# Performance work log

Measured on AMD Instinct MI355X. Metric: run time of the kernel, lower is better.

Reference implementation:

```python
import jax, jax.numpy as jnp
import numpy as np

B_SZ = 1
SEQ = 4096
IN_DIM = 1024
D_MODEL = 512
D_INNER = 1024   # expand(2) * d_model
D_STATE = 16
D_CONV = 4
DT_RANK = 32     # ceil(d_model / 16)
N_LAYERS = 2
N_CLASSES = 2


def setup_inputs() -> dict:
    key = jax.random.key(0)
    ks = jax.random.split(key, 12)
    s = 0.02
    x = jax.random.normal(ks[0], (B_SZ, SEQ, IN_DIM), jnp.float32)
    fc1_w = jax.random.normal(ks[1], (D_MODEL, IN_DIM), jnp.float32) * s
    fc1_b = jnp.zeros((D_MODEL,), jnp.float32)
    ln_w = jnp.ones((N_LAYERS, D_MODEL), jnp.float32)
    ln_b = jnp.zeros((N_LAYERS, D_MODEL), jnp.float32)
    in_proj_w = jax.random.normal(ks[2], (N_LAYERS, 2 * D_INNER, D_MODEL), jnp.float32) * s
    conv_w = jax.random.normal(ks[3], (N_LAYERS, D_INNER, D_CONV), jnp.float32) * 0.1
    conv_b = jnp.zeros((N_LAYERS, D_INNER), jnp.float32)
    x_proj_w = jax.random.normal(ks[4], (N_LAYERS, DT_RANK + 2 * D_STATE, D_INNER), jnp.float32) * s
    dt_proj_w = jax.random.normal(ks[5], (N_LAYERS, D_INNER, DT_RANK), jnp.float32) * s
    # bias so softplus(bias) ~ 0.01 (typical dt init)
    dt_proj_b = jnp.full((N_LAYERS, D_INNER), float(np.log(np.expm1(0.01))), jnp.float32)
    A_log = jnp.broadcast_to(jnp.log(jnp.arange(1, D_STATE + 1, dtype=jnp.float32)),
                             (N_LAYERS, D_INNER, D_STATE)).copy()
    D_skip = jnp.ones((N_LAYERS, D_INNER), jnp.float32)
    norm_w = jnp.ones((D_MODEL,), jnp.float32)
    norm_b = jnp.zeros((D_MODEL,), jnp.float32)
    cls_w = jax.random.normal(ks[6], (N_CLASSES, D_MODEL), jnp.float32) * s
    cls_b = jnp.zeros((N_CLASSES,), jnp.float32)
    return {"x": x, "fc1_w": fc1_w, "fc1_b": fc1_b, "ln_w": ln_w, "ln_b": ln_b,
            "in_proj_w": in_proj_w, "conv_w": conv_w, "conv_b": conv_b,
            "x_proj_w": x_proj_w, "dt_proj_w": dt_proj_w, "dt_proj_b": dt_proj_b,
            "A_log": A_log, "D_skip": D_skip, "norm_w": norm_w, "norm_b": norm_b,
            "cls_w": cls_w, "cls_b": cls_b}


def layernorm(h, w, b, eps=1e-5):
    mu = h.mean(-1, keepdims=True)
    var = ((h - mu) ** 2).mean(-1, keepdims=True)
    return (h - mu) * jax.lax.rsqrt(var + eps) * w + b


def mamba_block(h, in_proj_w, conv_w, conv_b, x_proj_w, dt_proj_w, dt_proj_b, A_log, D_skip):
    # h: [B, L, d_model]
    xz = jnp.einsum('bld,ed->ble', h, in_proj_w)          # [B, L, 2*D_INNER]
    xc, z = jnp.split(xz, 2, axis=-1)                     # each [B, L, D_INNER]
    # causal depthwise conv along L (kernel D_CONV)
    xp = jnp.pad(xc, ((0, 0), (D_CONV - 1, 0), (0, 0)))
    conv = sum(xp[:, k:k + xc.shape[1], :] * conv_w[:, k] for k in range(D_CONV))
    xc = jax.nn.silu(conv + conv_b)
    dbc = jnp.einsum('bld,ed->ble', xc, x_proj_w)         # [B, L, DT_RANK + 2*N]
    dt = jax.nn.softplus(jnp.einsum('blr,dr->bld', dbc[..., :DT_RANK], dt_proj_w) + dt_proj_b)
    Bm = dbc[..., DT_RANK:DT_RANK + D_STATE]              # [B, L, N]
    Cm = dbc[..., DT_RANK + D_STATE:]                     # [B, L, N]
    A = -jnp.exp(A_log)                                   # [D_INNER, N]
    dA = jnp.exp(dt[..., None] * A)                       # [B, L, D_INNER, N]
    dBx = dt[..., None] * Bm[:, :, None, :] * xc[..., None]

    def step(s, ins):
        dA_t, dBx_t, C_t = ins
        s = dA_t * s + dBx_t                              # [B, D_INNER, N]
        y = jnp.einsum('bdn,bn->bd', s, C_t)
        return s, y

    s0 = jnp.zeros((h.shape[0], D_INNER, D_STATE), h.dtype)
    _, ys = jax.lax.scan(step, s0, (dA.transpose(1, 0, 2, 3),
                                    dBx.transpose(1, 0, 2, 3),
                                    Cm.transpose(1, 0, 2)))
    y = ys.transpose(1, 0, 2) + xc * D_skip               # [B, L, D_INNER]
    y = y * jax.nn.silu(z)
    return y


def reference(x, fc1_w, fc1_b, ln_w, ln_b, in_proj_w, conv_w, conv_b,
              x_proj_w, dt_proj_w, dt_proj_b, A_log, D_skip,
              norm_w, norm_b, cls_w, cls_b):
    # out_proj of each Mamba layer folded: out_proj_w stored in in_proj? No -> build here.
    # We use the last N_LAYERS rows trick not needed: out projection is d_inner->d_model,
    # reuse in_proj_w transposed halves would be unfaithful, so derive deterministic weights.
    out_proj_w = jnp.stack([
        jax.random.normal(jax.random.fold_in(jax.random.key(7), i),
                          (D_MODEL, D_INNER), jnp.float32) * 0.02
        for i in range(N_LAYERS)])
    h = jax.nn.gelu(jnp.einsum('bli,di->bld', x, fc1_w) + fc1_b)
    for i in range(N_LAYERS):
        res = h
        hn = layernorm(h, ln_w[i], ln_b[i])
        y = mamba_block(hn, in_proj_w[i], conv_w[i], conv_b[i], x_proj_w[i],
                        dt_proj_w[i], dt_proj_b[i], A_log[i], D_skip[i])
        h = jnp.einsum('ble,de->bld', y, out_proj_w[i]) + res
    h = layernorm(h, norm_w, norm_b)
    hidden = h.mean(axis=1)                               # avg aggregation
    pred = hidden @ cls_w.T + cls_b
    return hidden, pred, h
```

## Files before the change

kernel.cpp:

```cpp
#include <hip/hip_runtime.h>
#include <cstdint>
#include <cstddef>

#define SEQ     4096
#define IN_DIM  1024
#define D_MODEL 512
#define D_INNER 1024
#define D_STATE 16
#define DT_RANK 32

#define CHUNK   32
#define NCHUNK  128
#define NREC    16384

#define LOG2E 1.44269504088896f

static const size_t OFF_H     = 0;
static const size_t OFF_PS    = 2097152;
static const size_t OFF_Z     = 6291456;
static const size_t OFF_XC    = 10485760;
static const size_t OFF_DT    = 14680064;
static const size_t OFF_CARRY = 18874368;
static const size_t OFF_HNB   = 20971520;
static const size_t OFF_FC1WB = 22020096;
static const size_t OFF_WIB   = 22282240;
static const size_t OFF_XPWB  = 23330816;
static const size_t OFF_DPWB  = 23396352;
static const size_t OFF_DBCF  = 23429120;
static const size_t OFF_DBCB  = 23691264;
static const size_t OFF_WOUTB = 23822336;
static const size_t OFF_PART  = 24346624;

typedef __attribute__((ext_vector_type(8))) short bf16x8;
typedef __attribute__((ext_vector_type(4))) float f32x4;

__device__ __forceinline__ uint32_t rotl32(uint32_t v, int r) { return (v << r) | (v >> (32 - r)); }

__device__ __forceinline__ void threefry2x32(uint32_t k0, uint32_t k1, uint32_t x0, uint32_t x1,
                                             uint32_t& o0, uint32_t& o1) {
  uint32_t ks0 = k0, ks1 = k1, ks2 = k0 ^ k1 ^ 0x1BD11BDAu;
  x0 += ks0; x1 += ks1;
  const int rotA[4] = {13, 15, 26, 6};
  const int rotB[4] = {17, 29, 16, 24};
  uint32_t ks[3] = {ks0, ks1, ks2};
#pragma unroll
  for (int r = 0; r < 5; ++r) {
    const int* rr = (r & 1) ? rotB : rotA;
#pragma unroll
    for (int j = 0; j < 4; ++j) { x0 += x1; x1 = rotl32(x1, rr[j]); x1 ^= x0; }
    x0 += ks[(r + 1) % 3];
    x1 += ks[(r + 2) % 3] + (uint32_t)(r + 1);
  }
  o0 = x0; o1 = x1;
}

__device__ __forceinline__ float erfinv32(float x) {
  float w = -log1pf(-x * x);
  float p;
  if (w < 5.0f) {
    w -= 2.5f;
    p = 2.81022636e-08f;
    p = fmaf(p, w, 3.43273939e-07f);
    p = fmaf(p, w, -3.5233877e-06f);
    p = fmaf(p, w, -4.39150654e-06f);
    p = fmaf(p, w, 0.00021858087f);
    p = fmaf(p, w, -0.00125372503f);
    p = fmaf(p, w, -0.00417768164f);
    p = fmaf(p, w, 0.246640727f);
    p = fmaf(p, w, 1.50140941f);
  } else {
    w = sqrtf(w) - 3.0f;
    p = -0.000200214257f;
    p = fmaf(p, w, 0.000100950558f);
    p = fmaf(p, w, 0.00134934322f);
    p = fmaf(p, w, -0.00367342844f);
    p = fmaf(p, w, 0.00573950773f);
    p = fmaf(p, w, -0.0076224613f);
    p = fmaf(p, w, 0.00943887047f);
    p = fmaf(p, w, 1.00167406f);
    p = fmaf(p, w, 2.83297682f);
  }
  return p * x;
}

__device__ __forceinline__ float bits_to_normal(uint32_t b) {
  float f = __uint_as_float((b >> 9) | 0x3f800000u) - 1.0f;
  const float lo = -0.99999994f;
  float u = f * (1.0f - lo) + lo;
  u = fmaxf(lo, u);
  return 1.41421356f * erfinv32(u);
}

__device__ __forceinline__ ushort f2bf(float x) {
  uint32_t u = __float_as_uint(x);
  u = (u + 0x7FFFu + ((u >> 16) & 1u)) >> 16;
  return (ushort)u;
}
__device__ __forceinline__ bf16x8 pack8(float4 a, float4 b) {
  bf16x8 v;
  v[0] = f2bf(a.x); v[1] = f2bf(a.y); v[2] = f2bf(a.z); v[3] = f2bf(a.w);
  v[4] = f2bf(b.x); v[5] = f2bf(b.y); v[6] = f2bf(b.z); v[7] = f2bf(b.w);
  return v;
}

__global__ __launch_bounds__(256) void gen_wout(ushort* __restrict__ w) {
  int gid = blockIdx.x * 256 + threadIdx.x;
  int layer = gid >> 19;
  int j = gid & 0x7FFFF;
  uint32_t k0, k1;
  threefry2x32(0u, 7u, 0u, (uint32_t)layer, k0, k1);
  uint32_t o0, o1;
  threefry2x32(k0, k1, 0u, (uint32_t)j, o0, o1);
  w[(size_t)layer * 524288 + j] = f2bf(bits_to_normal(o0 ^ o1) * 0.02f);
}

__global__ __launch_bounds__(256) void convert_all(
    const float* __restrict__ x,   const float* __restrict__ fc1w,
    const float* __restrict__ ipw, const float* __restrict__ xpw,
    const float* __restrict__ dpw,
    ushort* __restrict__ xb, ushort* __restrict__ fc1wb, ushort* __restrict__ ipwb,
    ushort* __restrict__ xpwb, ushort* __restrict__ dpwb) {
  int gid = blockIdx.x * 256 + threadIdx.x;
  const float* src; ushort* dst; size_t off;
  if (gid < 524288)      { src = x;    dst = xb;    off = gid; }
  else if (gid < 589824) { src = fc1w; dst = fc1wb; off = gid - 524288; }
  else if (gid < 851968) { src = ipw;  dst = ipwb;  off = gid - 589824; }
  else if (gid < 868352) { src = xpw;  dst = xpwb;  off = gid - 851968; }
  else if (gid < 876544) { src = dpw;  dst = dpwb;  off = gid - 868352; }
  else return;
  const float4* p = (const float4*)(src + off * 8);
  *(bf16x8*)(dst + off * 8) = pack8(p[0], p[1]);
}

__device__ __forceinline__ float silu_f(float v) { return v / (1.0f + exp2f(-LOG2E * v)); }
__device__ __forceinline__ float gelu_f(float v) {
  float v3 = v * v * v;
  return 0.5f * v * (1.0f + tanhf(0.7978845608028654f * (v + 0.044715f * v3)));
}
__device__ __forceinline__ float softplus_f(float v) {
  return fmaxf(v, 0.0f) + log1pf(exp2f(-LOG2E * fabsf(v)));
}

enum { EPI_NONE = 0, EPI_BIAS_GELU = 1, EPI_INPROJ = 2, EPI_SOFTPLUS = 3, EPI_RESID = 4, EPI_DBC = 5 };

template <int EPI, int NT>
__global__ __launch_bounds__(256) void gemm_bf(
    const ushort* __restrict__ A, int lda,
    const ushort* __restrict__ B, int ldb,
    float* __restrict__ C, int ldc, int K,
    const float* __restrict__ bias, float* __restrict__ out2,
    ushort* __restrict__ outb) {
  constexpr int NB = NT / 64;
  __shared__ ushort As[2][64][40];
  __shared__ ushort Bs[2][NT][40];
  const int m0 = blockIdx.y * 64, n0 = blockIdx.x * NT;
  const int tid = threadIdx.x;
  const int arow = tid >> 2, ach = (tid & 3) * 8;
  const int lane = tid & 63, wid = tid >> 6;
  const int lr = lane & 15, lhi = lane >> 4;
  const ushort* Ap  = A + (size_t)(m0 + arow) * lda + ach;
  const ushort* Bp0 = B + (size_t)(n0 + arow) * ldb + ach;
  const ushort* Bp1 = (NB > 1) ? (B + (size_t)(n0 + 64 + arow) * ldb + ach) : Bp0;

  f32x4 acc[NT / 16] = {};
  uint4 ra, rb0, rb1;

  ra  = *(const uint4*)Ap;
  rb0 = *(const uint4*)Bp0;
  if (NB > 1) rb1 = *(const uint4*)Bp1;
  *(uint4*)&As[0][arow][ach] = ra;
  *(uint4*)&Bs[0][arow][ach] = rb0;
  if (NB > 1) *(uint4*)&Bs[0][64 + arow][ach] = rb1;
  __syncthreads();

  const int nk = K >> 5;
  int cur = 0;
  for (int ki = 0; ki < nk; ++ki) {
    const bool more = (ki + 1 < nk);
    if (more) {
      const int k = (ki + 1) << 5;
      ra  = *(const uint4*)(Ap + k);
      rb0 = *(const uint4*)(Bp0 + k);
      if (NB > 1) rb1 = *(const uint4*)(Bp1 + k);
    }
    bf16x8 af = *(const bf16x8*)&As[cur][wid * 16 + lr][lhi * 8];
#pragma unroll
    for (int t = 0; t < NT / 16; ++t) {
      bf16x8 bv = *(const bf16x8*)&Bs[cur][t * 16 + lr][lhi * 8];
      acc[t] = __builtin_amdgcn_mfma_f32_16x16x32_bf16(af, bv, acc[t], 0, 0, 0);
    }
    if (more) {
      *(uint4*)&As[cur ^ 1][arow][ach] = ra;
      *(uint4*)&Bs[cur ^ 1][arow][ach] = rb0;
      if (NB > 1) *(uint4*)&Bs[cur ^ 1][64 + arow][ach] = rb1;
    }
    __syncthreads();
    cur ^= 1;
  }

#pragma unroll
  for (int t = 0; t < NT / 16; ++t) {
    const int n = n0 + t * 16 + lr;
#pragma unroll
    for (int r = 0; r < 4; ++r) {
      const int m = m0 + wid * 16 + lhi * 4 + r;
      float v = acc[t][r];
      if (EPI == EPI_NONE) {
        C[(size_t)m * ldc + n] = v;
      } else if (EPI == EPI_BIAS_GELU) {
        v += bias[n];
        C[(size_t)m * ldc + n] = gelu_f(v);
      } else if (EPI == EPI_SOFTPLUS) {
        v += bias[n];
        C[(size_t)m * ldc + n] = softplus_f(v);
      } else if (EPI == EPI_RESID) {
        C[(size_t)m * ldc + n] += v;
      } else if (EPI == EPI_INPROJ) {
        if (n < D_INNER) C[(size_t)m * D_INNER + n] = v;
        else             out2[(size_t)m * D_INNER + (n - D_INNER)] = silu_f(v);
      } else if (EPI == EPI_DBC) {
        C[(size_t)m * 64 + n] = v;
        outb[(size_t)m * 64 + n] = f2bf(v);
      }
    }
  }
}

template <int EPI>
__global__ __launch_bounds__(256) void gemm_bf128(
    const ushort* __restrict__ A, int lda,
    const ushort* __restrict__ B, int ldb,
    float* __restrict__ C, int ldc, int K,
    const float* __restrict__ bias, float* __restrict__ out2) {
  __shared__ ushort As[2][128][40];
  __shared__ ushort Bs[2][128][40];
  const int m0 = blockIdx.y * 128, n0 = blockIdx.x * 128;
  const int tid = threadIdx.x;
  const int lane = tid & 63, wid = tid >> 6;
  const int lr = lane & 15, lhi = lane >> 4;
  const int r0_ = tid >> 2, ach = (tid & 3) * 8;
  const ushort* Ap0 = A + (size_t)(m0 + r0_) * lda + ach;
  const ushort* Ap1 = A + (size_t)(m0 + r0_ + 64) * lda + ach;
  const ushort* Bp0 = B + (size_t)(n0 + r0_) * ldb + ach;
  const ushort* Bp1 = B + (size_t)(n0 + r0_ + 64) * ldb + ach;

  f32x4 acc[16] = {};
  uint4 ra0, ra1, rb0, rb1;

  ra0 = *(const uint4*)Ap0; ra1 = *(const uint4*)Ap1;
  rb0 = *(const uint4*)Bp0; rb1 = *(const uint4*)Bp1;
  *(uint4*)&As[0][r0_][ach] = ra0; *(uint4*)&As[0][r0_ + 64][ach] = ra1;
  *(uint4*)&Bs[0][r0_][ach] = rb0; *(uint4*)&Bs[0][r0_ + 64][ach] = rb1;
  __syncthreads();

  const int nk = K >> 5;
  int cur = 0;
  for (int ki = 0; ki < nk; ++ki) {
    const bool more = (ki + 1 < nk);
    if (more) {
      const int k = (ki + 1) << 5;
      ra0 = *(const uint4*)(Ap0 + k); ra1 = *(const uint4*)(Ap1 + k);
      rb0 = *(const uint4*)(Bp0 + k); rb1 = *(const uint4*)(Bp1 + k);
    }
    bf16x8 af0 = *(const bf16x8*)&As[cur][wid * 32 + lr][lhi * 8];
    bf16x8 af1 = *(const bf16x8*)&As[cur][wid * 32 + 16 + lr][lhi * 8];
#pragma unroll
    for (int t = 0; t < 8; ++t) {
      bf16x8 bv = *(const bf16x8*)&Bs[cur][t * 16 + lr][lhi * 8];
      acc[t]     = __builtin_amdgcn_mfma_f32_16x16x32_bf16(af0, bv, acc[t], 0, 0, 0);
      acc[8 + t] = __builtin_amdgcn_mfma_f32_16x16x32_bf16(af1, bv, acc[8 + t], 0, 0, 0);
    }
    if (more) {
      *(uint4*)&As[cur ^ 1][r0_][ach] = ra0; *(uint4*)&As[cur ^ 1][r0_ + 64][ach] = ra1;
      *(uint4*)&Bs[cur ^ 1][r0_][ach] = rb0; *(uint4*)&Bs[cur ^ 1][r0_ + 64][ach] = rb1;
    }
    __syncthreads();
    cur ^= 1;
  }

#pragma unroll
  for (int fr = 0; fr < 2; ++fr) {
#pragma unroll
    for (int t = 0; t < 8; ++t) {
      const int n = n0 + t * 16 + lr;
#pragma unroll
      for (int r = 0; r < 4; ++r) {
        const int m = m0 + wid * 32 + fr * 16 + lhi * 4 + r;
        float v = acc[fr * 8 + t][r];
        if (EPI == EPI_INPROJ) {
          if (n < D_INNER) C[(size_t)m * D_INNER + n] = v;
          else             out2[(size_t)m * D_INNER + (n - D_INNER)] = silu_f(v);
        } else {
          C[(size_t)m * ldc + n] = v;
        }
      }
    }
  }
}

template <int BF>
__global__ __launch_bounds__(256) void ln_rows(const float* __restrict__ in,
                                               const float* __restrict__ w,
                                               const float* __restrict__ b,
                                               float* __restrict__ outf,
                                               ushort* __restrict__ outb) {
  __shared__ double red[4];
  const int row = blockIdx.x, t = threadIdx.x;
  const float* r = in + (size_t)row * D_MODEL;
  double x0 = (double)r[t], x1 = (double)r[t + 256];
  double s = x0 + x1;
#pragma unroll
  for (int o = 32; o >= 1; o >>= 1) s += __shfl_down(s, o);
  int wid = t >> 6, lane = t & 63;
  if (lane == 0) red[wid] = s;
  __syncthreads();
  double mu = (red[0] + red[1] + red[2] + red[3]) * (1.0 / 512.0);
  __syncthreads();
  double d0 = x0 - mu, d1 = x1 - mu;
  double v = d0 * d0 + d1 * d1;
#pragma unroll
  for (int o = 32; o >= 1; o >>= 1) v += __shfl_down(v, o);
  if (lane == 0) red[wid] = v;
  __syncthreads();
  double var = (red[0] + red[1] + red[2] + red[3]) * (1.0 / 512.0);
  double rs = rsqrt(var + 1e-5);
  float o0 = (float)(d0 * rs * (double)w[t] + (double)b[t]);
  float o1 = (float)(d1 * rs * (double)w[t + 256] + (double)b[t + 256]);
  if (BF) {
    outb[(size_t)row * D_MODEL + t]       = f2bf(o0);
    outb[(size_t)row * D_MODEL + t + 256] = f2bf(o1);
  } else {
    outf[(size_t)row * D_MODEL + t]       = o0;
    outf[(size_t)row * D_MODEL + t + 256] = o1;
  }
}

__global__ __launch_bounds__(256) void conv_silu2(const float* __restrict__ xcr,
                                                  const float* __restrict__ cw,
                                                  const float* __restrict__ cb,
                                                  float* __restrict__ outf,
                                                  ushort* __restrict__ outb) {
  const int l = blockIdx.x;
  for (int q = 0; q < 4; ++q) {
    const int d = threadIdx.x + q * 256;
    float acc = cb[d];
#pragma unroll
    for (int k = 0; k < 4; ++k) {
      const int ll = l + k - 3;
      const float xv = (ll >= 0) ? xcr[(size_t)ll * D_INNER + d] : 0.0f;
      acc = fmaf(xv, cw[d * 4 + k], acc);
    }
    float o = silu_f(acc);
    outf[(size_t)l * D_INNER + d] = o;
    outb[(size_t)l * D_INNER + d] = f2bf(o);
  }
}

__global__ __launch_bounds__(256) void scanA(const float* __restrict__ dt,
                                             const float* __restrict__ dbc,
                                             const float* __restrict__ xc,
                                             const float* __restrict__ Alog,
                                             float* __restrict__ P, float* __restrict__ S) {
  const int c = blockIdx.y;
  const int d = blockIdx.x * 256 + threadIdx.x;
  float a2[16], s[16];
#pragma unroll
  for (int q = 0; q < 4; ++q) {
    float4 al = *(const float4*)(Alog + (size_t)d * 16 + q * 4);
    a2[4*q+0] = -expf(al.x) * LOG2E; a2[4*q+1] = -expf(al.y) * LOG2E;
    a2[4*q+2] = -expf(al.z) * LOG2E; a2[4*q+3] = -expf(al.w) * LOG2E;
  }
#pragma unroll
  for (int n = 0; n < 16; ++n) s[n] = 0.0f;
  float sdt = 0.0f;
  const int l0 = c * CHUNK;
#pragma unroll 2
  for (int t = 0; t < CHUNK; ++t) {
    const int l = l0 + t;
    const float dtv = dt[(size_t)l * D_INNER + d];
    const float xv  = xc[(size_t)l * D_INNER + d];
    const float dx = dtv * xv;
    sdt += dtv;
    float bv[16];
    const float4* B4 = (const float4*)(dbc + (size_t)l * 64 + DT_RANK);
    *(float4*)&bv[0]  = B4[0]; *(float4*)&bv[4]  = B4[1];
    *(float4*)&bv[8]  = B4[2]; *(float4*)&bv[12] = B4[3];
#pragma unroll
    for (int n = 0; n < 16; ++n)
      s[n] = fmaf(exp2f(dtv * a2[n]), s[n], bv[n] * dx);
  }
  float4* Sp = (float4*)(S + (size_t)c * NREC + (size_t)d * 16);
  float4* Pp = (float4*)(P + (size_t)c * NREC + (size_t)d * 16);
#pragma unroll
  for (int q = 0; q < 4; ++q) {
    Sp[q] = make_float4(s[4*q], s[4*q+1], s[4*q+2], s[4*q+3]);
    Pp[q] = make_float4(exp2f(a2[4*q]*sdt), exp2f(a2[4*q+1]*sdt),
                        exp2f(a2[4*q+2]*sdt), exp2f(a2[4*q+3]*sdt));
  }
}

__global__ __launch_bounds__(256) void scanB(const float* __restrict__ P,
                                             const float* __restrict__ S,
                                             float* __restrict__ carry) {
  int idx = blockIdx.x * 256 + threadIdx.x;
  float cr = 0.0f;
  for (int c = 0; c < NCHUNK; ++c) {
    size_t k = (size_t)c * NREC + idx;
    carry[k] = cr;
    cr = fmaf(P[k], cr, S[k]);
  }
}

__global__ __launch_bounds__(256) void scanC(const float* __restrict__ dt,
                                             const float* __restrict__ dbc,
                                             const float* __restrict__ xc,
                                             const float* __restrict__ Alog,
                                             const float* __restrict__ carry,
                                             const float* __restrict__ Dskip,
                                             const float* __restrict__ zs,
                                             ushort* __restrict__ yb) {
  const int c = blockIdx.y;
  const int d = blockIdx.x * 256 + threadIdx.x;
  float a2[16], s[16];
#pragma unroll
  for (int q = 0; q < 4; ++q) {
    float4 al = *(const float4*)(Alog + (size_t)d * 16 + q * 4);
    a2[4*q+0] = -expf(al.x) * LOG2E; a2[4*q+1] = -expf(al.y) * LOG2E;
    a2[4*q+2] = -expf(al.z) * LOG2E; a2[4*q+3] = -expf(al.w) * LOG2E;
    float4 cr = *(const float4*)(carry + (size_t)c * NREC + (size_t)d * 16 + q * 4);
    s[4*q+0] = cr.x; s[4*q+1] = cr.y; s[4*q+2] = cr.z; s[4*q+3] = cr.w;
  }
  const float dsk = Dskip[d];
  const int l0 = c * CHUNK;
#pragma unroll 2
  for (int t = 0; t < CHUNK; ++t) {
    const int l = l0 + t;
    const float dtv = dt[(size_t)l * D_INNER + d];
    const float xv  = xc[(size_t)l * D_INNER + d];
    const float dx = dtv * xv;
    float bv[16], cv[16];
    const float4* B4 = (const float4*)(dbc + (size_t)l * 64 + DT_RANK);
    *(float4*)&bv[0]  = B4[0]; *(float4*)&bv[4]  = B4[1];
    *(float4*)&bv[8]  = B4[2]; *(float4*)&bv[12] = B4[3];
    *(float4*)&cv[0]  = B4[4]; *(float4*)&cv[4]  = B4[5];
    *(float4*)&cv[8]  = B4[6]; *(float4*)&cv[12] = B4[7];
    float acc = 0.0f;
#pragma unroll
    for (int n = 0; n < 16; ++n) {
      s[n] = fmaf(exp2f(dtv * a2[n]), s[n], bv[n] * dx);
      acc = fmaf(s[n], cv[n], acc);
    }
    float yv = fmaf(xv, dsk, acc);
    yb[(size_t)l * D_INNER + d] = f2bf(yv * zs[(size_t)l * D_INNER + d]);
  }
}

__global__ __launch_bounds__(512) void colsum(const float* __restrict__ h, double* __restrict__ part) {
  int d = threadIdx.x;
  int r0 = blockIdx.x * 128;
  double s = 0.0;
  for (int r = 0; r < 128; ++r) s += (double)h[(size_t)(r0 + r) * D_MODEL + d];
  part[blockIdx.x * D_MODEL + d] = s;
}

__global__ __launch_bounds__(512) void head_k(const double* __restrict__ part,
                                              const float* __restrict__ cls_w,
                                              const float* __restrict__ cls_b,
                                              float* __restrict__ out) {
  __shared__ double l0[512], l1[512];
  int d = threadIdx.x;
  double s = 0.0;
  for (int b = 0; b < 32; ++b) s += part[b * D_MODEL + d];
  double hv = s * (1.0 / 4096.0);
  out[d] = (float)hv;
  l0[d] = hv * (double)cls_w[d];
  l1[d] = hv * (double)cls_w[D_MODEL + d];
  __syncthreads();
  for (int o = 256; o > 0; o >>= 1) {
    if (d < o) { l0[d] += l0[d + o]; l1[d] += l1[d + o]; }
    __syncthreads();
  }
  if (d == 0) { out[512] = (float)(l0[0] + (double)cls_b[0]); out[513] = (float)(l1[0] + (double)cls_b[1]); }
}

extern "C" void kernel_launch(void* const* d_in, const int* in_sizes, int n_in,
                              void* d_out, int out_size, void* d_ws, size_t ws_size,
                              hipStream_t stream) {
  const float* x         = (const float*)d_in[0];
  const float* fc1_w     = (const float*)d_in[1];
  const float* fc1_b     = (const float*)d_in[2];
  const float* ln_w      = (const float*)d_in[3];
  const float* ln_b      = (const float*)d_in[4];
  const float* in_proj_w = (const float*)d_in[5];
  const float* conv_w    = (const float*)d_in[6];
  const float* conv_b    = (const float*)d_in[7];
  const float* x_proj_w  = (const float*)d_in[8];
  const float* dt_proj_w = (const float*)d_in[9];
  const float* dt_proj_b = (const float*)d_in[10];
  const float* A_log     = (const float*)d_in[11];
  const float* D_skip    = (const float*)d_in[12];
  const float* norm_w    = (const float*)d_in[13];
  const float* norm_b    = (const float*)d_in[14];
  const float* cls_w     = (const float*)d_in[15];
  const float* cls_b     = (const float*)d_in[16];
  float* out = (float*)d_out;
  float* ws  = (float*)d_ws;

  float*  h_buf   = ws + OFF_H;
  float*  xcraw   = ws + OFF_PS;
  float*  P_buf   = ws + OFF_PS;
  float*  S_buf   = ws + OFF_PS + 2097152;
  ushort* y_bf    = (ushort*)(ws + OFF_PS);
  float*  z_buf   = ws + OFF_Z;
  float*  xc_buf  = ws + OFF_XC;
  float*  dt_buf  = ws + OFF_DT;
  ushort* x_bf    = (ushort*)(ws + OFF_DT);
  ushort* xc_bf   = (ushort*)(ws + OFF_DT);
  float*  carry_b = ws + OFF_CARRY;
  ushort* hn_bf   = (ushort*)(ws + OFF_HNB);
  ushort* fc1w_bf = (ushort*)(ws + OFF_FC1WB);
  ushort* Wi_bf   = (ushort*)(ws + OFF_WIB);
  ushort* xpw_bf  = (ushort*)(ws + OFF_XPWB);
  ushort* dpw_bf  = (ushort*)(ws + OFF_DPWB);
  float*  dbc_f   = ws + OFF_DBCF;
  ushort* dbc_bf  = (ushort*)(ws + OFF_DBCB);
  ushort* wout_bf = (ushort*)(ws + OFF_WOUTB);
  double* part    = (double*)(ws + OFF_PART);

  gen_wout<<<4096, 256, 0, stream>>>(wout_bf);
  convert_all<<<3424, 256, 0, stream>>>(x, fc1_w, in_proj_w, x_proj_w, dt_proj_w,
                                        x_bf, fc1w_bf, Wi_bf, xpw_bf, dpw_bf);

  gemm_bf<EPI_BIAS_GELU, 128><<<dim3(4, 64), 256, 0, stream>>>(
      x_bf, IN_DIM, fc1w_bf, IN_DIM, h_buf, D_MODEL, IN_DIM, fc1_b, nullptr, nullptr);

  for (int i = 0; i < 2; ++i) {
    ln_rows<1><<<4096, 256, 0, stream>>>(h_buf, ln_w + i * D_MODEL, ln_b + i * D_MODEL,
                                         nullptr, hn_bf);
    gemm_bf128<EPI_INPROJ><<<dim3(16, 32), 256, 0, stream>>>(
        hn_bf, D_MODEL, Wi_bf + (size_t)i * 1048576, D_MODEL, xcraw, D_INNER, D_MODEL,
        nullptr, z_buf);
    conv_silu2<<<4096, 256, 0, stream>>>(xcraw, conv_w + (size_t)i * D_INNER * 4,
                                         conv_b + i * D_INNER, xc_buf, xc_bf);
    gemm_bf<EPI_DBC, 64><<<dim3(1, 64), 256, 0, stream>>>(
        xc_bf, D_INNER, xpw_bf + (size_t)i * 65536, D_INNER, dbc_f, 64, D_INNER,
        nullptr, nullptr, dbc_bf);
    gemm_bf<EPI_SOFTPLUS, 128><<<dim3(8, 64), 256, 0, stream>>>(
        dbc_bf, 64, dpw_bf + (size_t)i * 32768, DT_RANK, dt_buf, D_INNER, DT_RANK,
        dt_proj_b + i * D_INNER, nullptr, nullptr);
    const float* Alog_i = A_log + (size_t)i * D_INNER * D_STATE;
    scanA<<<dim3(4, NCHUNK), 256, 0, stream>>>(dt_buf, dbc_f, xc_buf, Alog_i, P_buf, S_buf);
    scanB<<<64, 256, 0, stream>>>(P_buf, S_buf, carry_b);
    scanC<<<dim3(4, NCHUNK), 256, 0, stream>>>(dt_buf, dbc_f, xc_buf, Alog_i, carry_b,
                                               D_skip + i * D_INNER, z_buf, y_bf);
    gemm_bf<EPI_RESID, 128><<<dim3(4, 64), 256, 0, stream>>>(
        y_bf, D_INNER, wout_bf + (size_t)i * 524288, D_INNER, h_buf, D_MODEL, D_INNER,
        nullptr, nullptr, nullptr);
  }

  ln_rows<0><<<4096, 256, 0, stream>>>(h_buf, norm_w, norm_b, out + 514, nullptr);
  colsum<<<32, 512, 0, stream>>>(out + 514, part);
  head_k<<<1, 512, 0, stream>>>(part, cls_w, cls_b, out);
}
```

Measured before the change: 384.7 us.

## Fuse conv into x_proj GEMM, recompute dt in scans, merge weight prep kernels

Merges the out-projection weight generation with the bf16 conversion kernel. Fuses the depthwise conv+SiLU into the x_proj GEMM's A-tile staging, and drops the dt_proj GEMM so each scan thread recomputes dt with a 32-wide dot product plus softplus from the fp32 dbc row. It also stores z as bf16 and moves the fc1 and out-projection GEMMs to the 128x128 tile kernel. This removes several launches and the dt/z fp32 round trips through memory, at the cost of redundant dt compute in both scan passes, only 64 blocks for the conv+x_proj kernel, and fewer blocks for the 128-tile GEMMs.

```diff
diff --git a/kernel.cpp b/kernel.cpp
--- a/kernel.cpp
+++ b/kernel.cpp
@@ -96,6 +96,9 @@
   u = (u + 0x7FFFu + ((u >> 16) & 1u)) >> 16;
   return (ushort)u;
 }
+__device__ __forceinline__ float bf2f(ushort u) {
+  return __uint_as_float(((uint32_t)u) << 16);
+}
 __device__ __forceinline__ bf16x8 pack8(float4 a, float4 b) {
   bf16x8 v;
   v[0] = f2bf(a.x); v[1] = f2bf(a.y); v[2] = f2bf(a.z); v[3] = f2bf(a.w);
@@ -103,30 +106,29 @@
   return v;
 }
 
-__global__ __launch_bounds__(256) void gen_wout(ushort* __restrict__ w) {
-  int gid = blockIdx.x * 256 + threadIdx.x;
-  int layer = gid >> 19;
-  int j = gid & 0x7FFFF;
-  uint32_t k0, k1;
-  threefry2x32(0u, 7u, 0u, (uint32_t)layer, k0, k1);
-  uint32_t o0, o1;
-  threefry2x32(k0, k1, 0u, (uint32_t)j, o0, o1);
-  w[(size_t)layer * 524288 + j] = f2bf(bits_to_normal(o0 ^ o1) * 0.02f);
-}
-
-__global__ __launch_bounds__(256) void convert_all(
+__global__ __launch_bounds__(256) void gen_convert(
     const float* __restrict__ x,   const float* __restrict__ fc1w,
     const float* __restrict__ ipw, const float* __restrict__ xpw,
-    const float* __restrict__ dpw,
+    ushort* __restrict__ woutb,
     ushort* __restrict__ xb, ushort* __restrict__ fc1wb, ushort* __restrict__ ipwb,
-    ushort* __restrict__ xpwb, ushort* __restrict__ dpwb) {
+    ushort* __restrict__ xpwb) {
   int gid = blockIdx.x * 256 + threadIdx.x;
+  if (gid < 1048576) {
+    int layer = gid >> 19;
+    int j = gid & 0x7FFFF;
+    uint32_t k0, k1;
+    threefry2x32(0u, 7u, 0u, (uint32_t)layer, k0, k1);
+    uint32_t o0, o1;
+    threefry2x32(k0, k1, 0u, (uint32_t)j, o0, o1);
+    woutb[(size_t)layer * 524288 + j] = f2bf(bits_to_normal(o0 ^ o1) * 0.02f);
+    return;
+  }
+  int g = gid - 1048576;
   const float* src; ushort* dst; size_t off;
-  if (gid < 524288)      { src = x;    dst = xb;    off = gid; }
-  else if (gid < 589824) { src = fc1w; dst = fc1wb; off = gid - 524288; }
-  else if (gid < 851968) { src = ipw;  dst = ipwb;  off = gid - 589824; }
-  else if (gid < 868352) { src = xpw;  dst = xpwb;  off = gid - 851968; }
-  else if (gid < 876544) { src = dpw;  dst = dpwb;  off = gid - 868352; }
+  if (g < 524288)      { src = x;    dst = xb;    off = g; }
+  else if (g < 589824) { src = fc1w; dst = fc1wb; off = g - 524288; }
+  else if (g < 851968) { src = ipw;  dst = ipwb;  off = g - 589824; }
+  else if (g < 868352) { src = xpw;  dst = xpwb;  off = g - 851968; }
   else return;
   const float4* p = (const float4*)(src + off * 8);
   *(bf16x8*)(dst + off * 8) = pack8(p[0], p[1]);
@@ -141,97 +143,14 @@
   return fmaxf(v, 0.0f) + log1pf(exp2f(-LOG2E * fabsf(v)));
 }
 
-enum { EPI_NONE = 0, EPI_BIAS_GELU = 1, EPI_INPROJ = 2, EPI_SOFTPLUS = 3, EPI_RESID = 4, EPI_DBC = 5 };
-
-template <int EPI, int NT>
-__global__ __launch_bounds__(256) void gemm_bf(
-    const ushort* __restrict__ A, int lda,
-    const ushort* __restrict__ B, int ldb,
-    float* __restrict__ C, int ldc, int K,
-    const float* __restrict__ bias, float* __restrict__ out2,
-    ushort* __restrict__ outb) {
-  constexpr int NB = NT / 64;
-  __shared__ ushort As[2][64][40];
-  __shared__ ushort Bs[2][NT][40];
-  const int m0 = blockIdx.y * 64, n0 = blockIdx.x * NT;
-  const int tid = threadIdx.x;
-  const int arow = tid >> 2, ach = (tid & 3) * 8;
-  const int lane = tid & 63, wid = tid >> 6;
-  const int lr = lane & 15, lhi = lane >> 4;
-  const ushort* Ap  = A + (size_t)(m0 + arow) * lda + ach;
-  const ushort* Bp0 = B + (size_t)(n0 + arow) * ldb + ach;
-  const ushort* Bp1 = (NB > 1) ? (B + (size_t)(n0 + 64 + arow) * ldb + ach) : Bp0;
-
-  f32x4 acc[NT / 16] = {};
-  uint4 ra, rb0, rb1;
-
-  ra  = *(const uint4*)Ap;
-  rb0 = *(const uint4*)Bp0;
-  if (NB > 1) rb1 = *(const uint4*)Bp1;
-  *(uint4*)&As[0][arow][ach] = ra;
-  *(uint4*)&Bs[0][arow][ach] = rb0;
-  if (NB > 1) *(uint4*)&Bs[0][64 + arow][ach] = rb1;
-  __syncthreads();
-
-  const int nk = K >> 5;
-  int cur = 0;
-  for (int ki = 0; ki < nk; ++ki) {
-    const bool more = (ki + 1 < nk);
-    if (more) {
-      const int k = (ki + 1) << 5;
-      ra  = *(const uint4*)(Ap + k);
-      rb0 = *(const uint4*)(Bp0 + k);
-      if (NB > 1) rb1 = *(const uint4*)(Bp1 + k);
-    }
-    bf16x8 af = *(const bf16x8*)&As[cur][wid * 16 + lr][lhi * 8];
-#pragma unroll
-    for (int t = 0; t < NT / 16; ++t) {
-      bf16x8 bv = *(const bf16x8*)&Bs[cur][t * 16 + lr][lhi * 8];
-      acc[t] = __builtin_amdgcn_mfma_f32_16x16x32_bf16(af, bv, acc[t], 0, 0, 0);
-    }
-    if (more) {
-      *(uint4*)&As[cur ^ 1][arow][ach] = ra;
-      *(uint4*)&Bs[cur ^ 1][arow][ach] = rb0;
-      if (NB > 1) *(uint4*)&Bs[cur ^ 1][64 + arow][ach] = rb1;
-    }
-    __syncthreads();
-    cur ^= 1;
-  }
-
-#pragma unroll
-  for (int t = 0; t < NT / 16; ++t) {
-    const int n = n0 + t * 16 + lr;
-#pragma unroll
-    for (int r = 0; r < 4; ++r) {
-      const int m = m0 + wid * 16 + lhi * 4 + r;
-      float v = acc[t][r];
-      if (EPI == EPI_NONE) {
-        C[(size_t)m * ldc + n] = v;
-      } else if (EPI == EPI_BIAS_GELU) {
-        v += bias[n];
-        C[(size_t)m * ldc + n] = gelu_f(v);
-      } else if (EPI == EPI_SOFTPLUS) {
-        v += bias[n];
-        C[(size_t)m * ldc + n] = softplus_f(v);
-      } else if (EPI == EPI_RESID) {
-        C[(size_t)m * ldc + n] += v;
-      } else if (EPI == EPI_INPROJ) {
-        if (n < D_INNER) C[(size_t)m * D_INNER + n] = v;
-        else             out2[(size_t)m * D_INNER + (n - D_INNER)] = silu_f(v);
-      } else if (EPI == EPI_DBC) {
-        C[(size_t)m * 64 + n] = v;
-        outb[(size_t)m * 64 + n] = f2bf(v);
-      }
-    }
-  }
-}
+enum { EPI_BIAS_GELU = 1, EPI_INPROJ = 2, EPI_RESID = 4 };
 
 template <int EPI>
 __global__ __launch_bounds__(256) void gemm_bf128(
     const ushort* __restrict__ A, int lda,
     const ushort* __restrict__ B, int ldb,
     float* __restrict__ C, int ldc, int K,
-    const float* __restrict__ bias, float* __restrict__ out2) {
+    const float* __restrict__ bias, ushort* __restrict__ out2) {
   __shared__ ushort As[2][128][40];
   __shared__ ushort Bs[2][128][40];
   const int m0 = blockIdx.y * 128, n0 = blockIdx.x * 128;
@@ -287,13 +206,104 @@
       for (int r = 0; r < 4; ++r) {
         const int m = m0 + wid * 32 + fr * 16 + lhi * 4 + r;
         float v = acc[fr * 8 + t][r];
-        if (EPI == EPI_INPROJ) {
+        if (EPI == EPI_BIAS_GELU) {
+          v += bias[n];
+          C[(size_t)m * ldc + n] = gelu_f(v);
+        } else if (EPI == EPI_RESID) {
+          C[(size_t)m * ldc + n] += v;
+        } else if (EPI == EPI_INPROJ) {
           if (n < D_INNER) C[(size_t)m * D_INNER + n] = v;
-          else             out2[(size_t)m * D_INNER + (n - D_INNER)] = silu_f(v);
-        } else {
-          C[(size_t)m * ldc + n] = v;
+          else             out2[(size_t)m * D_INNER + (n - D_INNER)] = f2bf(silu_f(v));
         }
       }
+    }
+  }
+}
+
+__global__ __launch_bounds__(256) void conv_dbc(
+    const float* __restrict__ xcr,
+    const float* __restrict__ cw,
+    const float* __restrict__ cb,
+    const ushort* __restrict__ Bw,
+    float* __restrict__ xcf,
+    float* __restrict__ C) {
+  __shared__ ushort As[2][64][40];
+  __shared__ ushort Bs[2][64][40];
+  const int m0 = blockIdx.x * 64;
+  const int tid = threadIdx.x;
+  const int arow = tid >> 2, ach = (tid & 3) * 8;
+  const int lane = tid & 63, wid = tid >> 6;
+  const int lr = lane & 15, lhi = lane >> 4;
+  const int l = m0 + arow;
+  const ushort* Bp = Bw + (size_t)arow * 1024 + ach;
+
+  f32x4 acc[4] = {};
+
+  auto stage = [&](int d0) -> bf16x8 {
+    float r0[8], r1[8], r2[8], r3[8];
+#pragma unroll
+    for (int k = 0; k < 4; ++k) {
+      float* rr = (k == 0) ? r0 : (k == 1) ? r1 : (k == 2) ? r2 : r3;
+      const int ll = l + k - 3;
+      if (ll >= 0) {
+        const float* p = xcr + (size_t)ll * D_INNER + d0;
+        *(float4*)&rr[0] = *(const float4*)p;
+        *(float4*)&rr[4] = *(const float4*)(p + 4);
+      } else {
+#pragma unroll
+        for (int j = 0; j < 8; ++j) rr[j] = 0.0f;
+      }
+    }
+    float o[8];
+#pragma unroll
+    for (int j = 0; j < 8; ++j) {
+      const float4 cwv = *(const float4*)(cw + (size_t)(d0 + j) * 4);
+      float a = cb[d0 + j];
+      a = fmaf(r0[j], cwv.x, a);
+      a = fmaf(r1[j], cwv.y, a);
+      a = fmaf(r2[j], cwv.z, a);
+      a = fmaf(r3[j], cwv.w, a);
+      o[j] = silu_f(a);
+    }
+    *(float4*)(xcf + (size_t)l * D_INNER + d0)     = *(float4*)&o[0];
+    *(float4*)(xcf + (size_t)l * D_INNER + d0 + 4) = *(float4*)&o[4];
+    return pack8(*(float4*)&o[0], *(float4*)&o[4]);
+  };
+
+  bf16x8 a_next = stage(ach);
+  uint4 b_next = *(const uint4*)Bp;
+  *(bf16x8*)&As[0][arow][ach] = a_next;
+  *(uint4*)&Bs[0][arow][ach] = b_next;
+  __syncthreads();
+
+  int cur = 0;
+  for (int ki = 0; ki < 32; ++ki) {
+    const bool more = (ki + 1 < 32);
+    if (more) {
+      a_next = stage((ki + 1) * 32 + ach);
+      b_next = *(const uint4*)(Bp + (ki + 1) * 32);
+    }
+    bf16x8 af = *(const bf16x8*)&As[cur][wid * 16 + lr][lhi * 8];
+#pragma unroll
+    for (int t = 0; t < 4; ++t) {
+      bf16x8 bv = *(const bf16x8*)&Bs[cur][t * 16 + lr][lhi * 8];
+      acc[t] = __builtin_amdgcn_mfma_f32_16x16x32_bf16(af, bv, acc[t], 0, 0, 0);
+    }
+    if (more) {
+      *(bf16x8*)&As[cur ^ 1][arow][ach] = a_next;
+      *(uint4*)&Bs[cur ^ 1][arow][ach] = b_next;
+    }
+    __syncthreads();
+    cur ^= 1;
+  }
+
+#pragma unroll
+  for (int t = 0; t < 4; ++t) {
+    const int n = t * 16 + lr;
+#pragma unroll
+    for (int r = 0; r < 4; ++r) {
+      const int m = m0 + wid * 16 + lhi * 4 + r;
+      C[(size_t)m * 64 + n] = acc[t][r];
     }
   }
 }
@@ -335,35 +345,19 @@
   }
 }
 
-__global__ __launch_bounds__(256) void conv_silu2(const float* __restrict__ xcr,
-                                                  const float* __restrict__ cw,
-                                                  const float* __restrict__ cb,
-                                                  float* __restrict__ outf,
-                                                  ushort* __restrict__ outb) {
-  const int l = blockIdx.x;
-  for (int q = 0; q < 4; ++q) {
-    const int d = threadIdx.x + q * 256;
-    float acc = cb[d];
-#pragma unroll
-    for (int k = 0; k < 4; ++k) {
-      const int ll = l + k - 3;
-      const float xv = (ll >= 0) ? xcr[(size_t)ll * D_INNER + d] : 0.0f;
-      acc = fmaf(xv, cw[d * 4 + k], acc);
-    }
-    float o = silu_f(acc);
-    outf[(size_t)l * D_INNER + d] = o;
-    outb[(size_t)l * D_INNER + d] = f2bf(o);
-  }
-}
-
-__global__ __launch_bounds__(256) void scanA(const float* __restrict__ dt,
-                                             const float* __restrict__ dbc,
+__global__ __launch_bounds__(256) void scanA(const float* __restrict__ dbc,
                                              const float* __restrict__ xc,
                                              const float* __restrict__ Alog,
+                                             const float* __restrict__ dpw,
+                                             const float* __restrict__ dtb,
                                              float* __restrict__ P, float* __restrict__ S) {
   const int c = blockIdx.y;
   const int d = blockIdx.x * 256 + threadIdx.x;
-  float a2[16], s[16];
+  float a2[16], s[16], w[32];
+#pragma unroll
+  for (int q = 0; q < 8; ++q)
+    *(float4*)&w[4 * q] = *(const float4*)(dpw + (size_t)d * 32 + 4 * q);
+  const float bias = dtb[d];
 #pragma unroll
   for (int q = 0; q < 4; ++q) {
     float4 al = *(const float4*)(Alog + (size_t)d * 16 + q * 4);
@@ -377,12 +371,19 @@
 #pragma unroll 2
   for (int t = 0; t < CHUNK; ++t) {
     const int l = l0 + t;
-    const float dtv = dt[(size_t)l * D_INNER + d];
-    const float xv  = xc[(size_t)l * D_INNER + d];
+    const float* row = dbc + (size_t)l * 64;
+    float dv[32];
+#pragma unroll
+    for (int q = 0; q < 8; ++q) *(float4*)&dv[4 * q] = *(const float4*)(row + 4 * q);
+    float dot = bias;
+#pragma unroll
+    for (int r = 0; r < 32; ++r) dot = fmaf(dv[r], w[r], dot);
+    const float dtv = softplus_f(dot);
+    const float xv = xc[(size_t)l * D_INNER + d];
     const float dx = dtv * xv;
     sdt += dtv;
     float bv[16];
-    const float4* B4 = (const float4*)(dbc + (size_t)l * 64 + DT_RANK);
+    const float4* B4 = (const float4*)(row + DT_RANK);
     *(float4*)&bv[0]  = B4[0]; *(float4*)&bv[4]  = B4[1];
     *(float4*)&bv[8]  = B4[2]; *(float4*)&bv[12] = B4[3];
 #pragma unroll
@@ -411,17 +412,22 @@
   }
 }
 
-__global__ __launch_bounds__(256) void scanC(const float* __restrict__ dt,
-                                             const float* __restrict__ dbc,
+__global__ __launch_bounds__(256) void scanC(const float* __restrict__ dbc,
                                              const float* __restrict__ xc,
                                              const float* __restrict__ Alog,
+                                             const float* __restrict__ dpw,
+                                             const float* __restrict__ dtb,
                                              const float* __restrict__ carry,
                                              const float* __restrict__ Dskip,
-                                             const float* __restrict__ zs,
+                                             const ushort* __restrict__ zb,
                                              ushort* __restrict__ yb) {
   const int c = blockIdx.y;
   const int d = blockIdx.x * 256 + threadIdx.x;
-  float a2[16], s[16];
+  float a2[16], s[16], w[32];
+#pragma unroll
+  for (int q = 0; q < 8; ++q)
+    *(float4*)&w[4 * q] = *(const float4*)(dpw + (size_t)d * 32 + 4 * q);
+  const float bias = dtb[d];
 #pragma unroll
   for (int q = 0; q < 4; ++q) {
     float4 al = *(const float4*)(Alog + (size_t)d * 16 + q * 4);
@@ -435,11 +441,18 @@
 #pragma unroll 2
   for (int t = 0; t < CHUNK; ++t) {
     const int l = l0 + t;
-    const float dtv = dt[(size_t)l * D_INNER + d];
-    const float xv  = xc[(size_t)l * D_INNER + d];
+    const float* row = dbc + (size_t)l * 64;
+    float dv[32];
+#pragma unroll
+    for (int q = 0; q < 8; ++q) *(float4*)&dv[4 * q] = *(const float4*)(row + 4 * q);
+    float dot = bias;
+#pragma unroll
+    for (int r = 0; r < 32; ++r) dot = fmaf(dv[r], w[r], dot);
+    const float dtv = softplus_f(dot);
+    const float xv = xc[(size_t)l * D_INNER + d];
     const float dx = dtv * xv;
     float bv[16], cv[16];
-    const float4* B4 = (const float4*)(dbc + (size_t)l * 64 + DT_RANK);
+    const float4* B4 = (const float4*)(row + DT_RANK);
     *(float4*)&bv[0]  = B4[0]; *(float4*)&bv[4]  = B4[1];
     *(float4*)&bv[8]  = B4[2]; *(float4*)&bv[12] = B4[3];
     *(float4*)&cv[0]  = B4[4]; *(float4*)&cv[4]  = B4[5];
@@ -451,7 +464,7 @@
       acc = fmaf(s[n], cv[n], acc);
     }
     float yv = fmaf(xv, dsk, acc);
-    yb[(size_t)l * D_INNER + d] = f2bf(yv * zs[(size_t)l * D_INNER + d]);
+    yb[(size_t)l * D_INNER + d] = f2bf(yv * bf2f(zb[(size_t)l * D_INNER + d]));
   }
 }
 
@@ -511,51 +524,44 @@
   float*  P_buf   = ws + OFF_PS;
   float*  S_buf   = ws + OFF_PS + 2097152;
   ushort* y_bf    = (ushort*)(ws + OFF_PS);
-  float*  z_buf   = ws + OFF_Z;
+  ushort* z_bf    = (ushort*)(ws + OFF_Z);
   float*  xc_buf  = ws + OFF_XC;
-  float*  dt_buf  = ws + OFF_DT;
   ushort* x_bf    = (ushort*)(ws + OFF_DT);
-  ushort* xc_bf   = (ushort*)(ws + OFF_DT);
   float*  carry_b = ws + OFF_CARRY;
   ushort* hn_bf   = (ushort*)(ws + OFF_HNB);
   ushort* fc1w_bf = (ushort*)(ws + OFF_FC1WB);
   ushort* Wi_bf   = (ushort*)(ws + OFF_WIB);
   ushort* xpw_bf  = (ushort*)(ws + OFF_XPWB);
-  ushort* dpw_bf  = (ushort*)(ws + OFF_DPWB);
   float*  dbc_f   = ws + OFF_DBCF;
-  ushort* dbc_bf  = (ushort*)(ws + OFF_DBCB);
   ushort* wout_bf = (ushort*)(ws + OFF_WOUTB);
   double* part    = (double*)(ws + OFF_PART);
 
-  gen_wout<<<4096, 256, 0, stream>>>(wout_bf);
-  convert_all<<<3424, 256, 0, stream>>>(x, fc1_w, in_proj_w, x_proj_w, dt_proj_w,
-                                        x_bf, fc1w_bf, Wi_bf, xpw_bf, dpw_bf);
-
-  gemm_bf<EPI_BIAS_GELU, 128><<<dim3(4, 64), 256, 0, stream>>>(
-      x_bf, IN_DIM, fc1w_bf, IN_DIM, h_buf, D_MODEL, IN_DIM, fc1_b, nullptr, nullptr);
+  gen_convert<<<7488, 256, 0, stream>>>(x, fc1_w, in_proj_w, x_proj_w,
+                                        wout_bf, x_bf, fc1w_bf, Wi_bf, xpw_bf);
+
+  gemm_bf128<EPI_BIAS_GELU><<<dim3(4, 32), 256, 0, stream>>>(
+      x_bf, IN_DIM, fc1w_bf, IN_DIM, h_buf, D_MODEL, IN_DIM, fc1_b, nullptr);
 
   for (int i = 0; i < 2; ++i) {
     ln_rows<1><<<4096, 256, 0, stream>>>(h_buf, ln_w + i * D_MODEL, ln_b + i * D_MODEL,
                                          nullptr, hn_bf);
     gemm_bf128<EPI_INPROJ><<<dim3(16, 32), 256, 0, stream>>>(
         hn_bf, D_MODEL, Wi_bf + (size_t)i * 1048576, D_MODEL, xcraw, D_INNER, D_MODEL,
-        nullptr, z_buf);
-    conv_silu2<<<4096, 256, 0, stream>>>(xcraw, conv_w + (size_t)i * D_INNER * 4,
-                                         conv_b + i * D_INNER, xc_buf, xc_bf);
-    gemm_bf<EPI_DBC, 64><<<dim3(1, 64), 256, 0, stream>>>(
-        xc_bf, D_INNER, xpw_bf + (size_t)i * 65536, D_INNER, dbc_f, 64, D_INNER,
-        nullptr, nullptr, dbc_bf);
-    gemm_bf<EPI_SOFTPLUS, 128><<<dim3(8, 64), 256, 0, stream>>>(
-        dbc_bf, 64, dpw_bf + (size_t)i * 32768, DT_RANK, dt_buf, D_INNER, DT_RANK,
-        dt_proj_b + i * D_INNER, nullptr, nullptr);
+        nullptr, z_bf);
+    conv_dbc<<<64, 256, 0, stream>>>(xcraw, conv_w + (size_t)i * D_INNER * 4,
+                                     conv_b + i * D_INNER, xpw_bf + (size_t)i * 65536,
+                                     xc_buf, dbc_f);
     const float* Alog_i = A_log + (size_t)i * D_INNER * D_STATE;
-    scanA<<<dim3(4, NCHUNK), 256, 0, stream>>>(dt_buf, dbc_f, xc_buf, Alog_i, P_buf, S_buf);
+    const float* dpw_i  = dt_proj_w + (size_t)i * D_INNER * DT_RANK;
+    const float* dtb_i  = dt_proj_b + (size_t)i * D_INNER;
+    scanA<<<dim3(4, NCHUNK), 256, 0, stream>>>(dbc_f, xc_buf, Alog_i, dpw_i, dtb_i,
+                                               P_buf, S_buf);
     scanB<<<64, 256, 0, stream>>>(P_buf, S_buf, carry_b);
-    scanC<<<dim3(4, NCHUNK), 256, 0, stream>>>(dt_buf, dbc_f, xc_buf, Alog_i, carry_b,
-                                               D_skip + i * D_INNER, z_buf, y_bf);
-    gemm_bf<EPI_RESID, 128><<<dim3(4, 64), 256, 0, stream>>>(
+    scanC<<<dim3(4, NCHUNK), 256, 0, stream>>>(dbc_f, xc_buf, Alog_i, dpw_i, dtb_i,
+                                               carry_b, D_skip + i * D_INNER, z_bf, y_bf);
+    gemm_bf128<EPI_RESID><<<dim3(4, 32), 256, 0, stream>>>(
         y_bf, D_INNER, wout_bf + (size_t)i * 524288, D_INNER, h_buf, D_MODEL, D_INNER,
-        nullptr, nullptr, nullptr);
+        nullptr, nullptr);
   }
 
   ln_rows<0><<<4096, 256, 0, stream>>>(h_buf, norm_w, norm_b, out + 514, nullptr);
```

Result: slower. 547.8 us (+42.4%).
